# Performance work log

Measured on AMD Instinct MI355X. Metric: run time of the kernel, lower is better.

## Reference

```python
import jax, jax.numpy as jnp
import numpy as np

ANNEAL = 0.01

def _tsig(x, temp=ANNEAL):
    # temperature sigmoid with +/-50 clipping as in the torch source
    return jax.nn.sigmoid(jnp.clip(x / temp, -50.0, 50.0))

def setup_inputs() -> dict:
    key = jax.random.key(0)
    k1, k2 = jax.random.split(key)
    N, D = 512, 512
    preds = jax.random.normal(k1, (N, D), dtype=jnp.float32)
    labels = jax.random.randint(k2, (N,), 0, 64, dtype=jnp.int64)
    return {"preds": preds, "labels": labels}

def reference(preds, labels):
    N = preds.shape[0]
    dtype = preds.dtype
    eye = jnp.eye(N, dtype=dtype)
    same = (labels[:, None] == labels[None, :]).astype(dtype)
    I_pos = same * (1.0 - eye)                      # positives excl. self
    sim_mat = preds @ preds.T                       # [N, N]
    # sim_diff[i, j, k] = sim_mat[i, k] - sim_mat[i, j]
    sim_sg = _tsig(sim_mat[:, None, :] - sim_mat[:, :, None]) * (1.0 - eye)[None, :, :]
    sim_all_rk = 1.0 + jnp.sum(sim_sg, axis=-1)     # [N, N]
    # sum_k sim_sg[i,j,k] * I_pos[i,k]
    pos_sum = jnp.einsum('ijk,ik->ij', sim_sg, I_pos)
    sim_pos_rk = eye + I_pos + I_pos * pos_sum      # [N, N]
    n_pos = jnp.sum(I_pos, axis=1) + 1.0            # [N]
    per_anchor = jnp.sum(sim_pos_rk / sim_all_rk, axis=1) / n_pos
    per_anchor = jnp.where(n_pos > 1.0, per_anchor, 0.0)  # skip anchors with no positives
    ap = jnp.sum(per_anchor) / N
    return 1.0 - ap
```

## Files before the change

### kernel.cpp

```cpp
#include <hip/hip_runtime.h>

#define NN 512
#define FMAGIC 0x5AD0F1A6u

__global__ __launch_bounds__(256) void sap_gemm(const float* __restrict__ P,
                                                float* __restrict__ S) {
    __shared__ float As[32][33];
    __shared__ float Bs[32][33];
    const int t  = threadIdx.x;
    const int tx = t & 15, ty = t >> 4;
    const int i0 = blockIdx.y * 32, j0 = blockIdx.x * 32;

    float acc00 = 0.f, acc01 = 0.f, acc10 = 0.f, acc11 = 0.f;

    const int lr = t >> 3;
    const int lc = (t & 7) * 4;

    for (int kt = 0; kt < NN; kt += 32) {
        float4 a = *(const float4*)&P[(i0 + lr) * NN + kt + lc];
        float4 b = *(const float4*)&P[(j0 + lr) * NN + kt + lc];
        As[lr][lc + 0] = a.x; As[lr][lc + 1] = a.y;
        As[lr][lc + 2] = a.z; As[lr][lc + 3] = a.w;
        Bs[lr][lc + 0] = b.x; Bs[lr][lc + 1] = b.y;
        Bs[lr][lc + 2] = b.z; Bs[lr][lc + 3] = b.w;
        __syncthreads();
#pragma unroll
        for (int kk = 0; kk < 32; kk++) {
            float a0 = As[2 * ty][kk],     a1 = As[2 * ty + 1][kk];
            float b0 = Bs[2 * tx][kk],     b1 = Bs[2 * tx + 1][kk];
            acc00 += a0 * b0; acc01 += a0 * b1;
            acc10 += a1 * b0; acc11 += a1 * b1;
        }
        __syncthreads();
    }
    const int i = i0 + 2 * ty, j = j0 + 2 * tx;
    S[i * NN + j]           = acc00;
    S[i * NN + j + 1]       = acc01;
    S[(i + 1) * NN + j]     = acc10;
    S[(i + 1) * NN + j + 1] = acc11;
}

__global__ __launch_bounds__(256) void sap_rows2(const float* __restrict__ S,
                                                 const int* __restrict__ labels,
                                                 unsigned* __restrict__ pa_bits,
                                                 unsigned* __restrict__ flags,
                                                 float* __restrict__ out) {
    __shared__ float srow[NN];
    __shared__ float posf[NN];
    __shared__ int   poslist[NN];
    __shared__ int   npos_cnt;
    __shared__ float wave_part[4];
    __shared__ float pa_out[2];
    __shared__ float sh[256];

    const int t = threadIdx.x;
    const int b = blockIdx.x;
    const int i0 = 2 * b;
    const int wave = t >> 6, lane = t & 63;
    const float C1   = 100.0f * 1.44269504088896340736f;
    const float CLIP = 50.0f  * 1.44269504088896340736f;

    for (int a = 0; a < 2; ++a) {
        const int i = i0 + a;
        __syncthreads();
        if (t == 0) npos_cnt = 0;
        if (t < 4) wave_part[t] = 0.f;
        __syncthreads();
        const int li = labels[i];
        for (int k = t; k < NN; k += 256) {
            srow[k] = S[i * NN + k];
            bool p  = (labels[k] == li) && (k != i);
            posf[k] = p ? 1.f : 0.f;
            if (p) { int idx = atomicAdd(&npos_cnt, 1); poslist[idx] = k; }
        }
        __syncthreads();

        const int cnt = npos_cnt;
        if (cnt == 0) {
            if (t == 0) pa_out[a] = 0.f;
            continue;
        }

        float acc = 0.f;
        for (int idx = wave; idx <= cnt; idx += 4) {
            const int   j   = (idx == cnt) ? i : poslist[idx];
            const float sij = srow[j];
            float sum_all = 0.f, sum_pos = 0.f;
#pragma unroll
            for (int kk = 0; kk < 8; kk++) {
                const int k = lane + (kk << 6);
                float y = (sij - srow[k]) * C1;
                y = fminf(fmaxf(y, -CLIP), CLIP);
                float tt = 1.0f / (1.0f + exp2f(y));
                if (k == j) tt = 0.f;
                sum_all += tt;
                sum_pos += tt * posf[k];
            }
#pragma unroll
            for (int off = 32; off; off >>= 1) {
                sum_all += __shfl_down(sum_all, off);
                sum_pos += __shfl_down(sum_pos, off);
            }
            if (lane == 0) {
                const float den = 1.0f + sum_all;
                acc += ((j == i) ? 1.0f : (1.0f + sum_pos)) / den;
            }
        }
        if (lane == 0) wave_part[wave] = acc;
        __syncthreads();
        if (t == 0) {
            pa_out[a] = (wave_part[0] + wave_part[1] + wave_part[2] + wave_part[3])
                      / (float)(cnt + 1);
        }
    }
    __syncthreads();

    if (t == 0) {
        __hip_atomic_store(&pa_bits[i0],     __float_as_uint(pa_out[0]),
                           __ATOMIC_RELAXED, __HIP_MEMORY_SCOPE_AGENT);
        __hip_atomic_store(&pa_bits[i0 + 1], __float_as_uint(pa_out[1]),
                           __ATOMIC_RELAXED, __HIP_MEMORY_SCOPE_AGENT);
        asm volatile("s_waitcnt vmcnt(0)" ::: "memory");
        __hip_atomic_store(&flags[b], FMAGIC,
                           __ATOMIC_RELAXED, __HIP_MEMORY_SCOPE_AGENT);
    }

    if (b != 0) return;

    while (__hip_atomic_load(&flags[t], __ATOMIC_RELAXED,
                             __HIP_MEMORY_SCOPE_AGENT) != FMAGIC)
        __builtin_amdgcn_s_sleep(8);
    __hip_atomic_store(&flags[t], 0u, __ATOMIC_RELAXED,
                       __HIP_MEMORY_SCOPE_AGENT);
    __syncthreads();

    {
        float v0 = __uint_as_float(__hip_atomic_load(&pa_bits[t], __ATOMIC_RELAXED,
                                                     __HIP_MEMORY_SCOPE_AGENT));
        float v1 = __uint_as_float(__hip_atomic_load(&pa_bits[t + 256], __ATOMIC_RELAXED,
                                                     __HIP_MEMORY_SCOPE_AGENT));
        sh[t] = v0 + v1;
    }
    __syncthreads();
    for (int s = 128; s; s >>= 1) {
        if (t < s) sh[t] += sh[t + s];
        __syncthreads();
    }
    if (t == 0) out[0] = 1.0f - sh[0] / (float)NN;
}

extern "C" void kernel_launch(void* const* d_in, const int* in_sizes, int n_in,
                              void* d_out, int out_size, void* d_ws, size_t ws_size,
                              hipStream_t stream) {
    const float* preds  = (const float*)d_in[0];
    const int*   labels = (const int*)d_in[1];
    float* out = (float*)d_out;

    float*    S       = (float*)d_ws;
    unsigned* pa_bits = (unsigned*)((float*)d_ws + NN * NN);
    unsigned* flags   = pa_bits + NN;

    dim3 ggrid(NN / 32, NN / 32);
    sap_gemm<<<ggrid, 256, 0, stream>>>(preds, S);
    sap_rows2<<<NN / 2, 256, 0, stream>>>(S, labels, pa_bits, flags, out);
}
```

Before: 82.29 us.

## Fuse GEMM and rank kernels into one launch with per-row-band flag sync

Merges the similarity GEMM and the per-anchor rank computation into a single kernel of 256 blocks. Each block computes one 32x32 tile of S, publishes it with agent-scope atomic stores and a flag, then waits only on the 16 tiles of its own row band before running the sigmoid ranking on its two rows. This is meant to remove the second kernel launch and the full grid-wide dependency between the two stages. In exchange it relies on all 256 blocks being co-resident to avoid deadlock, and it adds spin-wait and atomic-load overhead.

After: 82.69 us. Within noise of the previous version (+0.5%).

```diff
diff --git a/kernel.cpp b/kernel.cpp
--- a/kernel.cpp
+++ b/kernel.cpp
@@ -2,49 +2,17 @@
 
 #define NN 512
 #define FMAGIC 0x5AD0F1A6u
+#define TMAGIC 0x3C96E5B1u
 
-__global__ __launch_bounds__(256) void sap_gemm(const float* __restrict__ P,
-                                                float* __restrict__ S) {
+__global__ __launch_bounds__(256) void sap_one(const float* __restrict__ P,
+                                               const int* __restrict__ labels,
+                                               unsigned* __restrict__ S_bits,
+                                               unsigned* __restrict__ tflags,
+                                               unsigned* __restrict__ pa_bits,
+                                               unsigned* __restrict__ pflags,
+                                               float* __restrict__ out) {
     __shared__ float As[32][33];
     __shared__ float Bs[32][33];
-    const int t  = threadIdx.x;
-    const int tx = t & 15, ty = t >> 4;
-    const int i0 = blockIdx.y * 32, j0 = blockIdx.x * 32;
-
-    float acc00 = 0.f, acc01 = 0.f, acc10 = 0.f, acc11 = 0.f;
-
-    const int lr = t >> 3;
-    const int lc = (t & 7) * 4;
-
-    for (int kt = 0; kt < NN; kt += 32) {
-        float4 a = *(const float4*)&P[(i0 + lr) * NN + kt + lc];
-        float4 b = *(const float4*)&P[(j0 + lr) * NN + kt + lc];
-        As[lr][lc + 0] = a.x; As[lr][lc + 1] = a.y;
-        As[lr][lc + 2] = a.z; As[lr][lc + 3] = a.w;
-        Bs[lr][lc + 0] = b.x; Bs[lr][lc + 1] = b.y;
-        Bs[lr][lc + 2] = b.z; Bs[lr][lc + 3] = b.w;
-        __syncthreads();
-#pragma unroll
-        for (int kk = 0; kk < 32; kk++) {
-            float a0 = As[2 * ty][kk],     a1 = As[2 * ty + 1][kk];
-            float b0 = Bs[2 * tx][kk],     b1 = Bs[2 * tx + 1][kk];
-            acc00 += a0 * b0; acc01 += a0 * b1;
-            acc10 += a1 * b0; acc11 += a1 * b1;
-        }
-        __syncthreads();
-    }
-    const int i = i0 + 2 * ty, j = j0 + 2 * tx;
-    S[i * NN + j]           = acc00;
-    S[i * NN + j + 1]       = acc01;
-    S[(i + 1) * NN + j]     = acc10;
-    S[(i + 1) * NN + j + 1] = acc11;
-}
-
-__global__ __launch_bounds__(256) void sap_rows2(const float* __restrict__ S,
-                                                 const int* __restrict__ labels,
-                                                 unsigned* __restrict__ pa_bits,
-                                                 unsigned* __restrict__ flags,
-                                                 float* __restrict__ out) {
     __shared__ float srow[NN];
     __shared__ float posf[NN];
     __shared__ int   poslist[NN];
@@ -55,20 +23,73 @@
 
     const int t = threadIdx.x;
     const int b = blockIdx.x;
-    const int i0 = 2 * b;
+
+    {
+        const int tx = t & 15, ty = t >> 4;
+        const int i0 = (b >> 4) * 32, j0 = (b & 15) * 32;
+        float acc00 = 0.f, acc01 = 0.f, acc10 = 0.f, acc11 = 0.f;
+        const int lr = t >> 3;
+        const int lc = (t & 7) * 4;
+
+        for (int kt = 0; kt < NN; kt += 32) {
+            float4 a  = *(const float4*)&P[(i0 + lr) * NN + kt + lc];
+            float4 bb = *(const float4*)&P[(j0 + lr) * NN + kt + lc];
+            As[lr][lc + 0] = a.x;  As[lr][lc + 1] = a.y;
+            As[lr][lc + 2] = a.z;  As[lr][lc + 3] = a.w;
+            Bs[lr][lc + 0] = bb.x; Bs[lr][lc + 1] = bb.y;
+            Bs[lr][lc + 2] = bb.z; Bs[lr][lc + 3] = bb.w;
+            __syncthreads();
+#pragma unroll
+            for (int kk = 0; kk < 32; kk++) {
+                float a0 = As[2 * ty][kk], a1 = As[2 * ty + 1][kk];
+                float b0 = Bs[2 * tx][kk], b1 = Bs[2 * tx + 1][kk];
+                acc00 += a0 * b0; acc01 += a0 * b1;
+                acc10 += a1 * b0; acc11 += a1 * b1;
+            }
+            __syncthreads();
+        }
+        const int i = i0 + 2 * ty, j = j0 + 2 * tx;
+        __hip_atomic_store(&S_bits[i * NN + j],           __float_as_uint(acc00),
+                           __ATOMIC_RELAXED, __HIP_MEMORY_SCOPE_AGENT);
+        __hip_atomic_store(&S_bits[i * NN + j + 1],       __float_as_uint(acc01),
+                           __ATOMIC_RELAXED, __HIP_MEMORY_SCOPE_AGENT);
+        __hip_atomic_store(&S_bits[(i + 1) * NN + j],     __float_as_uint(acc10),
+                           __ATOMIC_RELAXED, __HIP_MEMORY_SCOPE_AGENT);
+        __hip_atomic_store(&S_bits[(i + 1) * NN + j + 1], __float_as_uint(acc11),
+                           __ATOMIC_RELAXED, __HIP_MEMORY_SCOPE_AGENT);
+        asm volatile("s_waitcnt vmcnt(0)" ::: "memory");
+        __syncthreads();
+        if (t == 0)
+            __hip_atomic_store(&tflags[b], TMAGIC,
+                               __ATOMIC_RELAXED, __HIP_MEMORY_SCOPE_AGENT);
+    }
+
+    {
+        const int grp16 = (b >> 4) * 16;
+        if (t < 16) {
+            while (__hip_atomic_load(&tflags[grp16 + t], __ATOMIC_RELAXED,
+                                     __HIP_MEMORY_SCOPE_AGENT) != TMAGIC)
+                __builtin_amdgcn_s_sleep(8);
+        }
+        __syncthreads();
+    }
+
+    const int i0a = 2 * b;
     const int wave = t >> 6, lane = t & 63;
     const float C1   = 100.0f * 1.44269504088896340736f;
     const float CLIP = 50.0f  * 1.44269504088896340736f;
 
     for (int a = 0; a < 2; ++a) {
-        const int i = i0 + a;
+        const int i = i0a + a;
         __syncthreads();
         if (t == 0) npos_cnt = 0;
         if (t < 4) wave_part[t] = 0.f;
         __syncthreads();
         const int li = labels[i];
         for (int k = t; k < NN; k += 256) {
-            srow[k] = S[i * NN + k];
+            srow[k] = __uint_as_float(
+                __hip_atomic_load(&S_bits[i * NN + k], __ATOMIC_RELAXED,
+                                  __HIP_MEMORY_SCOPE_AGENT));
             bool p  = (labels[k] == li) && (k != i);
             posf[k] = p ? 1.f : 0.f;
             if (p) { int idx = atomicAdd(&npos_cnt, 1); poslist[idx] = k; }
@@ -116,22 +137,22 @@
     __syncthreads();
 
     if (t == 0) {
-        __hip_atomic_store(&pa_bits[i0],     __float_as_uint(pa_out[0]),
+        __hip_atomic_store(&pa_bits[i0a],     __float_as_uint(pa_out[0]),
                            __ATOMIC_RELAXED, __HIP_MEMORY_SCOPE_AGENT);
-        __hip_atomic_store(&pa_bits[i0 + 1], __float_as_uint(pa_out[1]),
+        __hip_atomic_store(&pa_bits[i0a + 1], __float_as_uint(pa_out[1]),
                            __ATOMIC_RELAXED, __HIP_MEMORY_SCOPE_AGENT);
         asm volatile("s_waitcnt vmcnt(0)" ::: "memory");
-        __hip_atomic_store(&flags[b], FMAGIC,
+        __hip_atomic_store(&pflags[b], FMAGIC,
                            __ATOMIC_RELAXED, __HIP_MEMORY_SCOPE_AGENT);
     }
 
     if (b != 0) return;
 
-    while (__hip_atomic_load(&flags[t], __ATOMIC_RELAXED,
+    while (__hip_atomic_load(&pflags[t], __ATOMIC_RELAXED,
                              __HIP_MEMORY_SCOPE_AGENT) != FMAGIC)
         __builtin_amdgcn_s_sleep(8);
-    __hip_atomic_store(&flags[t], 0u, __ATOMIC_RELAXED,
-                       __HIP_MEMORY_SCOPE_AGENT);
+    __hip_atomic_store(&pflags[t], 0u, __ATOMIC_RELAXED, __HIP_MEMORY_SCOPE_AGENT);
+    __hip_atomic_store(&tflags[t], 0u, __ATOMIC_RELAXED, __HIP_MEMORY_SCOPE_AGENT);
     __syncthreads();
 
     {
@@ -156,11 +177,11 @@
     const int*   labels = (const int*)d_in[1];
     float* out = (float*)d_out;
 
-    float*    S       = (float*)d_ws;
-    unsigned* pa_bits = (unsigned*)((float*)d_ws + NN * NN);
-    unsigned* flags   = pa_bits + NN;
+    unsigned* S_bits  = (unsigned*)d_ws;
+    unsigned* tflags  = S_bits + NN * NN;
+    unsigned* pa_bits = tflags + 256;
+    unsigned* pflags  = pa_bits + NN;
 
-    dim3 ggrid(NN / 32, NN / 32);
-    sap_gemm<<<ggrid, 256, 0, stream>>>(preds, S);
-    sap_rows2<<<NN / 2, 256, 0, stream>>>(S, labels, pa_bits, flags, out);
+    sap_one<<<256, 256, 0, stream>>>(preds, labels, S_bits, tflags,
+                                     pa_bits, pflags, out);
 }
```
